# Kernel tuning notes

Measured on AMD Instinct MI355X. Metric: run time of the kernel, lower is better.

Reference implementation:

```python
import jax, jax.numpy as jnp
import numpy as np

B, M, L, LQ, E, V = 32, 100, 30, 30, 256, 32000


def position_encoding(seq_len, emb):
    # faithful to MemN2N position encoding: 1 + 4*(k - (E+1)/2)*(j - (J+1)/2)/(E*J)
    j = jnp.arange(1, seq_len + 1, dtype=jnp.float32)[:, None]   # (J,1)
    k = jnp.arange(1, emb + 1, dtype=jnp.float32)[None, :]       # (1,E)
    half_e = (emb + 1) / 2.0
    half_j = (seq_len + 1) / 2.0
    return 1.0 + 4.0 * (k - half_e) * (j - half_j) / (emb * seq_len)  # (J,E)


def masked_softmax(x, m):
    xm = jnp.where(m > 0, x, -1e30)
    e = jnp.exp(xm - jnp.max(xm, axis=-1, keepdims=True)) * m
    return e / (jnp.sum(e, axis=-1, keepdims=True) + 1e-13)


def masked_log_softmax(x, m):
    return jax.nn.log_softmax(x + jnp.log(m + 1e-13), axis=-1)


def _forward(trainS, trainQ, trainVM, trainPM, trainSM, trainQM,
             A1, A2, A3, A4, W, b, gamma, beta):
    # query encoding: embed + position encode + query mask + sum over words
    Q = trainQ[:, 0, :]                                   # (B,LQ)
    pe_q = position_encoding(LQ, E)                       # (LQ,E)
    u = jnp.sum(A1[Q] * pe_q * trainQM[:, :, None], axis=1)  # (B,E)

    # story memory embeddings: gather + PE + sum over words.
    # NOTE: original code multiplies by trainSM but discards the result (bug),
    # so SM is intentionally NOT applied here.
    pe_s = position_encoding(L, E)                        # (L,E)
    embA1 = jnp.sum(A1[trainS] * pe_s, axis=2)            # (B,M,E)
    embA2 = jnp.sum(A2[trainS] * pe_s, axis=2)
    embA3 = jnp.sum(A3[trainS] * pe_s, axis=2)
    embA4 = jnp.sum(A4[trainS] * pe_s, axis=2)

    def hop(memA, memC, u):
        # scores = sum_E(memA * u) * PM (PM applied pre-sum is equivalent)
        scores = jnp.einsum('bme,be->bm', memA, u) * trainPM
        p = masked_softmax(scores, trainPM)               # (B,M)
        o = jnp.einsum('bm,bme->be', p, memC)             # (B,E)
        return o + u

    u = hop(embA1, embA2, u)   # hop 1
    u = hop(embA2, embA3, u)   # hop 2
    u = hop(embA3, embA4, u)   # hop 3

    # final linear + BatchNorm1d (training-mode batch stats, eps=1e-5)
    wx = u @ W.T + b                                      # (B,V)
    mean = jnp.mean(wx, axis=0)
    var = jnp.mean((wx - mean) ** 2, axis=0)
    y = gamma * (wx - mean) / jnp.sqrt(var + 1e-5) + beta
    return masked_log_softmax(y, trainVM)


def setup_inputs() -> dict:
    key = jax.random.key(0)
    ks = jax.random.split(key, 8)
    inp = {
        'trainS': jax.random.randint(ks[0], (B, M, L), 0, V, dtype=jnp.int32),
        'trainQ': jax.random.randint(ks[1], (B, 1, LQ), 0, V, dtype=jnp.int32),
        'trainVM': jnp.ones((B, V), jnp.float32),
        'trainPM': jnp.ones((B, M), jnp.float32),
        'trainSM': jnp.ones((B, M, L), jnp.float32),
        'trainQM': jnp.ones((B, LQ), jnp.float32),
        'A1': 0.1 * jax.random.normal(ks[2], (V, E), jnp.float32),
        'A2': 0.1 * jax.random.normal(ks[3], (V, E), jnp.float32),
        'A3': 0.1 * jax.random.normal(ks[4], (V, E), jnp.float32),
        'A4': 0.1 * jax.random.normal(ks[5], (V, E), jnp.float32),
        'W': jax.random.normal(ks[6], (V, E), jnp.float32) / np.sqrt(E),
        'b': jnp.zeros((V,), jnp.float32),
        'gamma': jnp.ones((V,), jnp.float32),
        'beta': jnp.zeros((V,), jnp.float32),
        'inspect': 0,
    }
    return inp


def reference(trainS, trainQ, trainVM, trainPM, trainSM, trainQM,
              A1, A2, A3, A4, W, b, gamma, beta, inspect):
    return _forward(trainS, trainQ, trainVM, trainPM, trainSM, trainQM,
                    A1, A2, A3, A4, W, b, gamma, beta)
```

## Files before the change

kernel.cpp:

```cpp
#include <hip/hip_runtime.h>
#include <math.h>

static constexpr int B_ = 32, M_ = 100, L_ = 30, LQ_ = 30, E_ = 256, V_ = 32000;

__global__ __launch_bounds__(256) void k_embed(const int* __restrict__ trainS,
                                               const float* __restrict__ A1,
                                               const float* __restrict__ A2,
                                               const float* __restrict__ A3,
                                               const float* __restrict__ A4,
                                               float* __restrict__ embA) {
    const int bm = blockIdx.x;
    const int tbl = threadIdx.x >> 6;
    const int e0 = (threadIdx.x & 63) * 4;
    const float* __restrict__ A = (tbl == 0) ? A1 : (tbl == 1) ? A2 : (tbl == 2) ? A3 : A4;
    const float half_e = (E_ + 1) * 0.5f;
    const float half_j = (L_ + 1) * 0.5f;
    const float inv = 1.0f / (float)(E_ * L_);
    const float k0 = (float)(e0 + 1) - half_e;
    const float k1 = k0 + 1.f, k2 = k0 + 2.f, k3 = k0 + 3.f;

    int idx[L_];
#pragma unroll
    for (int l = 0; l < L_; ++l) idx[l] = trainS[bm * L_ + l];

    float4 acc = make_float4(0.f, 0.f, 0.f, 0.f);
#pragma unroll
    for (int c = 0; c < 2; ++c) {
        float4 r[15];
#pragma unroll
        for (int j = 0; j < 15; ++j)
            r[j] = *reinterpret_cast<const float4*>(A + (size_t)idx[c * 15 + j] * E_ + e0);
        __builtin_amdgcn_sched_barrier(0);
#pragma unroll
        for (int j = 0; j < 15; ++j) {
            const int l = c * 15 + j;
            const float coef = 4.0f * ((float)(l + 1) - half_j) * inv;
            acc.x += r[j].x * (1.0f + coef * k0);
            acc.y += r[j].y * (1.0f + coef * k1);
            acc.z += r[j].z * (1.0f + coef * k2);
            acc.w += r[j].w * (1.0f + coef * k3);
        }
    }
    *reinterpret_cast<float4*>(embA + (size_t)tbl * (B_ * M_ * E_) + (size_t)bm * E_ + e0) = acc;
}

__global__ __launch_bounds__(1024) void k_hops(const int* __restrict__ trainQ,
                                               const float* __restrict__ trainQM,
                                               const float* __restrict__ A1,
                                               const float* __restrict__ embA,
                                               const float* __restrict__ trainPM,
                                               float* __restrict__ u_T,
                                               float* __restrict__ partial) {
    const int b = blockIdx.x;
    const int tid = threadIdx.x;
    const int lane = tid & 63;
    const int wave = tid >> 6;
    const int g = tid >> 8;
    const int e = tid & 255;
    if (tid < 8) partial[b * 8 + tid] = 0.f;
    __shared__ float u_sh[E_];
    __shared__ float sc[M_];
    __shared__ float p_sh[M_];
    __shared__ float osum[4][E_];

    {
        const float half_e = (E_ + 1) * 0.5f;
        const float half_j = (LQ_ + 1) * 0.5f;
        const float inv = 1.0f / (float)(E_ * LQ_);
        const float ke = (float)(e + 1) - half_e;
        const int l0 = g * 8;
        const int ln = (LQ_ - l0 < 8) ? (LQ_ - l0) : 8;
        int qi[8];
        float qm[8];
#pragma unroll
        for (int j = 0; j < 8; ++j) {
            if (j < ln) {
                qi[j] = trainQ[b * LQ_ + l0 + j];
                qm[j] = trainQM[b * LQ_ + l0 + j];
            } else { qi[j] = 0; qm[j] = 0.f; }
        }
        float r[8];
#pragma unroll
        for (int j = 0; j < 8; ++j)
            r[j] = (j < ln) ? A1[(size_t)qi[j] * E_ + e] : 0.f;
        float part = 0.f;
#pragma unroll
        for (int j = 0; j < 8; ++j) {
            const float pe = 1.0f + 4.0f * ke * ((float)(l0 + j + 1) - half_j) * inv;
            part += r[j] * pe * qm[j];
        }
        osum[g][e] = part;
    }
    __syncthreads();
    if (tid < E_) u_sh[tid] = osum[0][tid] + osum[1][tid] + osum[2][tid] + osum[3][tid];
    __syncthreads();

    for (int hop = 0; hop < 3; ++hop) {
        const float* memA = embA + (size_t)hop * (B_ * M_ * E_) + (size_t)b * M_ * E_;
        const float* memC = memA + (size_t)(B_ * M_ * E_);
#pragma unroll 2
        for (int m = wave; m < M_; m += 16) {
            const float* row = memA + m * E_;
            float part = 0.f;
#pragma unroll
            for (int j = 0; j < 4; ++j)
                part += row[lane + 64 * j] * u_sh[lane + 64 * j];
#pragma unroll
            for (int off = 32; off > 0; off >>= 1)
                part += __shfl_xor(part, off, 64);
            if (lane == 0) sc[m] = part * trainPM[b * M_ + m];
        }
        __syncthreads();
        if (wave == 0) {
            const float pm0 = (lane < M_) ? trainPM[b * M_ + lane] : 0.f;
            const float pm1 = (lane + 64 < M_) ? trainPM[b * M_ + lane + 64] : 0.f;
            const float x0 = (lane < M_ && pm0 > 0.f) ? sc[lane] : -1e30f;
            const float x1 = (lane + 64 < M_ && pm1 > 0.f) ? sc[lane + 64] : -1e30f;
            float mx = fmaxf(x0, x1);
#pragma unroll
            for (int off = 32; off > 0; off >>= 1)
                mx = fmaxf(mx, __shfl_xor(mx, off, 64));
            const float e0v = (lane < M_) ? expf(x0 - mx) * pm0 : 0.f;
            const float e1v = (lane + 64 < M_) ? expf(x1 - mx) * pm1 : 0.f;
            float ssum = e0v + e1v;
#pragma unroll
            for (int off = 32; off > 0; off >>= 1)
                ssum += __shfl_xor(ssum, off, 64);
            const float invs = 1.0f / (ssum + 1e-13f);
            if (lane < M_) p_sh[lane] = e0v * invs;
            if (lane + 64 < M_) p_sh[lane + 64] = e1v * invs;
        }
        __syncthreads();
        {
            float acc = 0.f;
            const float* crow = memC + e;
            const int m0 = g * 25;
#pragma unroll 5
            for (int mm = 0; mm < 25; ++mm)
                acc += p_sh[m0 + mm] * crow[(size_t)(m0 + mm) * E_];
            osum[g][e] = acc;
        }
        __syncthreads();
        if (tid < E_) u_sh[tid] += osum[0][tid] + osum[1][tid] + osum[2][tid] + osum[3][tid];
        __syncthreads();
    }
    if (tid < E_) u_T[tid * B_ + b] = u_sh[tid];
}

__global__ __launch_bounds__(256) void k_output(const float* __restrict__ u_T,
                                                const float* __restrict__ Wm,
                                                const float* __restrict__ bias,
                                                const float* __restrict__ gamma,
                                                const float* __restrict__ beta,
                                                const float* __restrict__ VM,
                                                float* __restrict__ z,
                                                float* __restrict__ partial) {
    __shared__ float u_lds[E_ * B_];
    __shared__ float pex[B_];
    const int tid = threadIdx.x;
    for (int i = tid; i < (E_ * B_) / 4; i += 256)
        reinterpret_cast<float4*>(u_lds)[i] = reinterpret_cast<const float4*>(u_T)[i];
    if (tid < B_) pex[tid] = 0.f;
    __syncthreads();

    const int bg = tid & 7;
    const int vl = tid >> 3;
    const int v = blockIdx.x * 32 + vl;
    const float* __restrict__ wr = Wm + (size_t)v * E_;

    float acc[4] = {0.f, 0.f, 0.f, 0.f};
    float4 wA[4], wB[4];
#pragma unroll
    for (int c = 0; c < 4; ++c) wA[c] = reinterpret_cast<const float4*>(wr)[c];

#pragma unroll 1
    for (int cc = 0; cc < 16; cc += 2) {
#pragma unroll
        for (int c = 0; c < 4; ++c) wB[c] = reinterpret_cast<const float4*>(wr)[(cc + 1) * 4 + c];
#pragma unroll
        for (int c = 0; c < 4; ++c) {
#pragma unroll
            for (int q = 0; q < 4; ++q) {
                const int e = cc * 16 + c * 4 + q;
                const float4 u4 = *reinterpret_cast<const float4*>(&u_lds[e * B_ + bg * 4]);
                const float w = (q == 0) ? wA[c].x : (q == 1) ? wA[c].y : (q == 2) ? wA[c].z : wA[c].w;
                acc[0] += w * u4.x; acc[1] += w * u4.y; acc[2] += w * u4.z; acc[3] += w * u4.w;
            }
        }
        if (cc + 2 < 16) {
#pragma unroll
            for (int c = 0; c < 4; ++c) wA[c] = reinterpret_cast<const float4*>(wr)[(cc + 2) * 4 + c];
        }
#pragma unroll
        for (int c = 0; c < 4; ++c) {
#pragma unroll
            for (int q = 0; q < 4; ++q) {
                const int e = (cc + 1) * 16 + c * 4 + q;
                const float4 u4 = *reinterpret_cast<const float4*>(&u_lds[e * B_ + bg * 4]);
                const float w = (q == 0) ? wB[c].x : (q == 1) ? wB[c].y : (q == 2) ? wB[c].z : wB[c].w;
                acc[0] += w * u4.x; acc[1] += w * u4.y; acc[2] += w * u4.z; acc[3] += w * u4.w;
            }
        }
    }

    const float bv = bias[v];
    float s1 = 0.f, s2 = 0.f;
#pragma unroll
    for (int i = 0; i < 4; ++i) {
        acc[i] += bv;
        s1 += acc[i];
        s2 += acc[i] * acc[i];
    }
#pragma unroll
    for (int off = 1; off < 8; off <<= 1) {
        s1 += __shfl_xor(s1, off, 64);
        s2 += __shfl_xor(s2, off, 64);
    }
    const float mean = s1 * (1.0f / B_);
    const float var = s2 * (1.0f / B_) - mean * mean;
    const float rstd = rsqrtf(var + 1e-5f);
    const float g = gamma[v], be = beta[v];

    float exs = 0.f;
    float ex[4];
#pragma unroll
    for (int i = 0; i < 4; ++i) {
        const int b = bg * 4 + i;
        const size_t row = (size_t)b * V_ + v;
        const float vm = VM[row] + 1e-13f;
        const float y = g * (acc[i] - mean) * rstd + be;
        z[row] = y + logf(vm);
        ex[i] = vm * expf(y);
    }
#pragma unroll
    for (int i = 0; i < 4; ++i)
        atomicAdd(&pex[bg * 4 + i], ex[i]);
    (void)exs;
    __syncthreads();
    if (tid < B_) atomicAdd(&partial[tid * 8 + (blockIdx.x & 7)], pex[tid]);
}

__global__ __launch_bounds__(256) void k_final(const float* __restrict__ z,
                                               const float* __restrict__ partial,
                                               float* __restrict__ out) {
    const int idx = blockIdx.x * 256 + threadIdx.x;
    const int b = idx / (V_ / 4);
    const int v4 = idx % (V_ / 4);
    float s = 0.f;
#pragma unroll
    for (int k = 0; k < 8; ++k) s += partial[b * 8 + k];
    const float lse = logf(s);
    const float4 x = reinterpret_cast<const float4*>(z + (size_t)b * V_)[v4];
    float4 o;
    o.x = x.x - lse; o.y = x.y - lse; o.z = x.z - lse; o.w = x.w - lse;
    reinterpret_cast<float4*>(out + (size_t)b * V_)[v4] = o;
}

extern "C" void kernel_launch(void* const* d_in, const int* in_sizes, int n_in,
                              void* d_out, int out_size, void* d_ws, size_t ws_size,
                              hipStream_t stream) {
    const int* trainS = (const int*)d_in[0];
    const int* trainQ = (const int*)d_in[1];
    const float* trainVM = (const float*)d_in[2];
    const float* trainPM = (const float*)d_in[3];
    const float* trainQM = (const float*)d_in[5];
    const float* A1 = (const float*)d_in[6];
    const float* A2 = (const float*)d_in[7];
    const float* A3 = (const float*)d_in[8];
    const float* A4 = (const float*)d_in[9];
    const float* Wm = (const float*)d_in[10];
    const float* bias = (const float*)d_in[11];
    const float* gamma = (const float*)d_in[12];
    const float* beta = (const float*)d_in[13];
    float* out = (float*)d_out;

    float* ws = (float*)d_ws;
    float* u_T = ws;
    float* embA = ws + 8192;
    float* z = embA + 4 * (B_ * M_ * E_);
    float* partial = z + (size_t)B_ * V_;

    k_embed<<<B_ * M_, 256, 0, stream>>>(trainS, A1, A2, A3, A4, embA);
    k_hops<<<B_, 1024, 0, stream>>>(trainQ, trainQM, A1, embA, trainPM, u_T, partial);
    k_output<<<V_ / 32, 256, 0, stream>>>(u_T, Wm, bias, gamma, beta, trainVM, z, partial);
    k_final<<<(B_ * V_ / 4) / 256, 256, 0, stream>>>(z, partial, out);
}
```

Measured before the change: 120.9 us.

## Compute output projection with bf16 MFMA and drop bias add

The output GEMM (u @ W.T) now runs on MFMA 16x16x32 bf16 instructions. u is stored row-major and converted to bf16 in a swizzled LDS layout, and W rows are converted to bf16 in registers. Each block now covers 64 vocab columns instead of 32. The bias add is removed, which is valid because training-mode BatchNorm subtracts the per-column mean and cancels any bias. Rounding inputs to bf16 costs precision in the logits.

```diff
diff --git a/kernel.cpp b/kernel.cpp
--- a/kernel.cpp
+++ b/kernel.cpp
@@ -2,6 +2,14 @@
 #include <math.h>
 
 static constexpr int B_ = 32, M_ = 100, L_ = 30, LQ_ = 30, E_ = 256, V_ = 32000;
+
+typedef __attribute__((ext_vector_type(8))) short bf16x8;
+typedef __attribute__((ext_vector_type(4))) float f32x4;
+
+__device__ __forceinline__ unsigned f2bf(float f) {
+    unsigned u = __float_as_uint(f);
+    return (u + 0x7FFFu + ((u >> 16) & 1u)) >> 16;
+}
 
 __global__ __launch_bounds__(256) void k_embed(const int* __restrict__ trainS,
                                                const float* __restrict__ A1,
@@ -49,7 +57,7 @@
                                                const float* __restrict__ A1,
                                                const float* __restrict__ embA,
                                                const float* __restrict__ trainPM,
-                                               float* __restrict__ u_T,
+                                               float* __restrict__ u_N,
                                                float* __restrict__ partial) {
     const int b = blockIdx.x;
     const int tid = threadIdx.x;
@@ -144,98 +152,112 @@
         if (tid < E_) u_sh[tid] += osum[0][tid] + osum[1][tid] + osum[2][tid] + osum[3][tid];
         __syncthreads();
     }
-    if (tid < E_) u_T[tid * B_ + b] = u_sh[tid];
-}
-
-__global__ __launch_bounds__(256) void k_output(const float* __restrict__ u_T,
+    if (tid < E_) u_N[b * E_ + tid] = u_sh[tid];
+}
+
+__global__ __launch_bounds__(256) void k_output(const float* __restrict__ u_N,
                                                 const float* __restrict__ Wm,
-                                                const float* __restrict__ bias,
                                                 const float* __restrict__ gamma,
                                                 const float* __restrict__ beta,
                                                 const float* __restrict__ VM,
                                                 float* __restrict__ z,
                                                 float* __restrict__ partial) {
-    __shared__ float u_lds[E_ * B_];
+    __shared__ char uAraw[32 * 512];
     __shared__ float pex[B_];
     const int tid = threadIdx.x;
-    for (int i = tid; i < (E_ * B_) / 4; i += 256)
-        reinterpret_cast<float4*>(u_lds)[i] = reinterpret_cast<const float4*>(u_T)[i];
+    {
+        const int m = tid >> 3;
+        const int kc = (tid & 7) * 32;
+        const float4* src = reinterpret_cast<const float4*>(u_N + m * E_ + kc);
+#pragma unroll
+        for (int j = 0; j < 4; ++j) {
+            const float4 f0 = src[2 * j];
+            const float4 f1 = src[2 * j + 1];
+            uint4 q;
+            q.x = f2bf(f0.x) | (f2bf(f0.y) << 16);
+            q.y = f2bf(f0.z) | (f2bf(f0.w) << 16);
+            q.z = f2bf(f1.x) | (f2bf(f1.y) << 16);
+            q.w = f2bf(f1.z) | (f2bf(f1.w) << 16);
+            const int k16 = kc / 8 + j;
+            const int off = m * 512 + ((k16 * 16) ^ ((m & 7) << 4));
+            *reinterpret_cast<uint4*>(uAraw + off) = q;
+        }
+    }
     if (tid < B_) pex[tid] = 0.f;
     __syncthreads();
 
-    const int bg = tid & 7;
-    const int vl = tid >> 3;
-    const int v = blockIdx.x * 32 + vl;
-    const float* __restrict__ wr = Wm + (size_t)v * E_;
-
-    float acc[4] = {0.f, 0.f, 0.f, 0.f};
-    float4 wA[4], wB[4];
-#pragma unroll
-    for (int c = 0; c < 4; ++c) wA[c] = reinterpret_cast<const float4*>(wr)[c];
-
-#pragma unroll 1
-    for (int cc = 0; cc < 16; cc += 2) {
-#pragma unroll
-        for (int c = 0; c < 4; ++c) wB[c] = reinterpret_cast<const float4*>(wr)[(cc + 1) * 4 + c];
-#pragma unroll
-        for (int c = 0; c < 4; ++c) {
-#pragma unroll
-            for (int q = 0; q < 4; ++q) {
-                const int e = cc * 16 + c * 4 + q;
-                const float4 u4 = *reinterpret_cast<const float4*>(&u_lds[e * B_ + bg * 4]);
-                const float w = (q == 0) ? wA[c].x : (q == 1) ? wA[c].y : (q == 2) ? wA[c].z : wA[c].w;
-                acc[0] += w * u4.x; acc[1] += w * u4.y; acc[2] += w * u4.z; acc[3] += w * u4.w;
-            }
-        }
-        if (cc + 2 < 16) {
-#pragma unroll
-            for (int c = 0; c < 4; ++c) wA[c] = reinterpret_cast<const float4*>(wr)[(cc + 2) * 4 + c];
-        }
-#pragma unroll
-        for (int c = 0; c < 4; ++c) {
-#pragma unroll
-            for (int q = 0; q < 4; ++q) {
-                const int e = (cc + 1) * 16 + c * 4 + q;
-                const float4 u4 = *reinterpret_cast<const float4*>(&u_lds[e * B_ + bg * 4]);
-                const float w = (q == 0) ? wB[c].x : (q == 1) ? wB[c].y : (q == 2) ? wB[c].z : wB[c].w;
-                acc[0] += w * u4.x; acc[1] += w * u4.y; acc[2] += w * u4.z; acc[3] += w * u4.w;
-            }
-        }
-    }
-
-    const float bv = bias[v];
+    const int lane = tid & 63;
+    const int wv = tid >> 6;
+    const int col = lane & 15;
+    const int grp = lane >> 4;
+    const int n0 = (blockIdx.x * 4 + wv) * 16;
+    const int v = n0 + col;
+
+    float4 wreg[16];
+    {
+        const float* wrow = Wm + (size_t)v * E_ + grp * 8;
+#pragma unroll
+        for (int s = 0; s < 8; ++s) {
+            wreg[2 * s] = *reinterpret_cast<const float4*>(wrow + s * 32);
+            wreg[2 * s + 1] = *reinterpret_cast<const float4*>(wrow + s * 32 + 4);
+        }
+    }
+    __builtin_amdgcn_sched_barrier(0);
+
+    bf16x8 af[2][8];
+#pragma unroll
+    for (int mt = 0; mt < 2; ++mt) {
+        const int m = mt * 16 + col;
+#pragma unroll
+        for (int s = 0; s < 8; ++s) {
+            const int k16 = s * 4 + grp;
+            const int off = m * 512 + ((k16 * 16) ^ ((m & 7) << 4));
+            af[mt][s] = *reinterpret_cast<bf16x8*>(uAraw + off);
+        }
+    }
+
+    f32x4 acc0 = {0.f, 0.f, 0.f, 0.f};
+    f32x4 acc1 = {0.f, 0.f, 0.f, 0.f};
+#pragma unroll
+    for (int s = 0; s < 8; ++s) {
+        const float4 w0 = wreg[2 * s], w1 = wreg[2 * s + 1];
+        bf16x8 bf;
+        bf[0] = (short)f2bf(w0.x); bf[1] = (short)f2bf(w0.y);
+        bf[2] = (short)f2bf(w0.z); bf[3] = (short)f2bf(w0.w);
+        bf[4] = (short)f2bf(w1.x); bf[5] = (short)f2bf(w1.y);
+        bf[6] = (short)f2bf(w1.z); bf[7] = (short)f2bf(w1.w);
+        acc0 = __builtin_amdgcn_mfma_f32_16x16x32_bf16(af[0][s], bf, acc0, 0, 0, 0);
+        acc1 = __builtin_amdgcn_mfma_f32_16x16x32_bf16(af[1][s], bf, acc1, 0, 0, 0);
+    }
+
     float s1 = 0.f, s2 = 0.f;
 #pragma unroll
-    for (int i = 0; i < 4; ++i) {
-        acc[i] += bv;
-        s1 += acc[i];
-        s2 += acc[i] * acc[i];
-    }
-#pragma unroll
-    for (int off = 1; off < 8; off <<= 1) {
-        s1 += __shfl_xor(s1, off, 64);
-        s2 += __shfl_xor(s2, off, 64);
-    }
+    for (int r = 0; r < 4; ++r) {
+        s1 += acc0[r] + acc1[r];
+        s2 += acc0[r] * acc0[r] + acc1[r] * acc1[r];
+    }
+    s1 += __shfl_xor(s1, 16, 64);
+    s2 += __shfl_xor(s2, 16, 64);
+    s1 += __shfl_xor(s1, 32, 64);
+    s2 += __shfl_xor(s2, 32, 64);
     const float mean = s1 * (1.0f / B_);
     const float var = s2 * (1.0f / B_) - mean * mean;
     const float rstd = rsqrtf(var + 1e-5f);
-    const float g = gamma[v], be = beta[v];
-
-    float exs = 0.f;
-    float ex[4];
-#pragma unroll
-    for (int i = 0; i < 4; ++i) {
-        const int b = bg * 4 + i;
-        const size_t row = (size_t)b * V_ + v;
-        const float vm = VM[row] + 1e-13f;
-        const float y = g * (acc[i] - mean) * rstd + be;
-        z[row] = y + logf(vm);
-        ex[i] = vm * expf(y);
-    }
-#pragma unroll
-    for (int i = 0; i < 4; ++i)
-        atomicAdd(&pex[bg * 4 + i], ex[i]);
-    (void)exs;
+    const float gg = gamma[v], be = beta[v];
+
+#pragma unroll
+    for (int mt = 0; mt < 2; ++mt) {
+#pragma unroll
+        for (int r = 0; r < 4; ++r) {
+            const int b = mt * 16 + grp * 4 + r;
+            const float wx = (mt == 0) ? acc0[r] : acc1[r];
+            const float y = gg * (wx - mean) * rstd + be;
+            const size_t row = (size_t)b * V_ + v;
+            const float vm = VM[row] + 1e-13f;
+            z[row] = y + logf(vm);
+            atomicAdd(&pex[b], vm * expf(y));
+        }
+    }
     __syncthreads();
     if (tid < B_) atomicAdd(&partial[tid * 8 + (blockIdx.x & 7)], pex[tid]);
 }
@@ -269,19 +291,18 @@
     const float* A3 = (const float*)d_in[8];
     const float* A4 = (const float*)d_in[9];
     const float* Wm = (const float*)d_in[10];
-    const float* bias = (const float*)d_in[11];
     const float* gamma = (const float*)d_in[12];
     const float* beta = (const float*)d_in[13];
     float* out = (float*)d_out;
 
     float* ws = (float*)d_ws;
-    float* u_T = ws;
+    float* u_N = ws;
     float* embA = ws + 8192;
     float* z = embA + 4 * (B_ * M_ * E_);
     float* partial = z + (size_t)B_ * V_;
 
     k_embed<<<B_ * M_, 256, 0, stream>>>(trainS, A1, A2, A3, A4, embA);
-    k_hops<<<B_, 1024, 0, stream>>>(trainQ, trainQM, A1, embA, trainPM, u_T, partial);
-    k_output<<<V_ / 32, 256, 0, stream>>>(u_T, Wm, bias, gamma, beta, trainVM, z, partial);
+    k_hops<<<B_, 1024, 0, stream>>>(trainQ, trainQM, A1, embA, trainPM, u_N, partial);
+    k_output<<<V_ / 64, 256, 0, stream>>>(u_N, Wm, gamma, beta, trainVM, z, partial);
     k_final<<<(B_ * V_ / 4) / 256, 256, 0, stream>>>(z, partial, out);
 }
```

Result: faster. 108.9 us (-9.9%).
